# Kernel tuning notes

Measured on AMD Instinct MI355X. Metric: run time of the kernel, lower is better.

The kernel has to match this reference:

```python
import jax, jax.numpy as jnp
import numpy as np

B, T, N, F, U, K = 64, 96, 64, 64, 64, 2
M = 2 * K + 1  # num_matrices = len(supports)*K + 1
NUM_CLASSES, NUM_PATIENT = 4, 50


def diffusion_conv(x, supports, W, b, K):
    # x: (B, N, Fin). Faithful to DiffusionGraphConv incl. x1,x0 = x2,x1 carryover.
    xs = [x]
    x0 = x
    for S in supports:
        x1 = jnp.einsum('mn,bnf->bmf', S, x0)
        xs.append(x1)
        for _ in range(2, K + 1):
            x2 = 2.0 * jnp.einsum('mn,bnf->bmf', S, x1) - x0
            xs.append(x2)
            x1, x0 = x2, x1
    Bv, Nv, Fv = x.shape
    xcat = jnp.stack(xs, axis=-1).reshape(Bv, Nv, Fv * len(xs))  # feature-major, matrix-minor
    return xcat @ W + b


def dcgru_step(x, h, supports, Wg, bg, Wc, bc, K, units):
    cat = jnp.concatenate([x, h], axis=-1)
    ru = jax.nn.sigmoid(diffusion_conv(cat, supports, Wg, bg, K))
    r, u = ru[..., :units], ru[..., units:]
    c = jnp.tanh(diffusion_conv(jnp.concatenate([x, r * h], axis=-1), supports, Wc, bc, K))
    return u * h + (1.0 - u) * c


def encoder(inputs, supports, layer_params, K, units):
    # inputs: (T, B, N, Fin); returns last-layer outputs over time (T, B, N, units)
    cur = inputs
    for (Wg, bg, Wc, bc) in layer_params:
        h0 = jnp.zeros((cur.shape[1], cur.shape[2], units), cur.dtype)
        def step(h, x, Wg=Wg, bg=bg, Wc=Wc, bc=bc):
            hn = dcgru_step(x, h, supports, Wg, bg, Wc, bc, K, units)
            return hn, hn
        _, cur = jax.lax.scan(step, h0, cur)
    return cur


def setup_inputs() -> dict:
    key = jax.random.key(0)
    ks = jax.random.split(key, 20)
    def w(k, shape):
        return (jax.random.normal(k, shape, dtype=jnp.float32) / np.sqrt(shape[0])).astype(jnp.float32)
    def rw(k):  # row-normalized random-walk support
        A = jax.random.uniform(k, (N, N), dtype=jnp.float32)
        return A / jnp.sum(A, axis=1, keepdims=True)
    in0 = F + U   # layer 0 concat(x, h)
    in1 = U + U   # layer 1
    inp = {
        'input_seq': jax.random.normal(ks[0], (B, T, N, F), dtype=jnp.float32),
        'seq_lengths': jax.random.randint(ks[1], (B,), 1, T + 1, dtype=jnp.int32),
        'support0': rw(ks[2]),
        'support1': rw(ks[3]),
        'Wg0': w(ks[4], (in0 * M, 2 * U)), 'bg0': jnp.ones((2 * U,), jnp.float32),
        'Wc0': w(ks[5], (in0 * M, U)),     'bc0': jnp.zeros((U,), jnp.float32),
        'Wg1': w(ks[6], (in1 * M, 2 * U)), 'bg1': jnp.ones((2 * U,), jnp.float32),
        'Wc1': w(ks[7], (in1 * M, U)),     'bc1': jnp.zeros((U,), jnp.float32),
        'fc_w': w(ks[8], (U, NUM_CLASSES)), 'fc_b': jnp.zeros((NUM_CLASSES,), jnp.float32),
        'id_w': w(ks[9], (U, NUM_PATIENT)), 'id_b': jnp.zeros((NUM_PATIENT,), jnp.float32),
    }
    return inp


def reference(input_seq, seq_lengths, support0, support1,
              Wg0, bg0, Wc0, bc0, Wg1, bg1, Wc1, bc1,
              fc_w, fc_b, id_w, id_b):
    supports = [support0, support1]
    layer_params = [(Wg0, bg0, Wc0, bc0), (Wg1, bg1, Wc1, bc1)]
    inputs = jnp.transpose(input_seq, (1, 0, 2, 3))        # (T, B, N, F)
    outs = encoder(inputs, supports, layer_params, K, U)    # (T, B, N, U)
    out_bt = jnp.transpose(outs, (1, 0, 2, 3))              # (B, T, N, U)
    last = out_bt[jnp.arange(out_bt.shape[0]), seq_lengths - 1]  # (B, N, U)
    h = jax.nn.relu(last)  # dropout is identity in eval
    pool_seizure = jnp.max(h @ fc_w + fc_b, axis=1)         # max over nodes -> (B, num_classes)
    pool_identity = jnp.max(h @ id_w + id_b, axis=1)        # (B, num_patient)
    return pool_seizure, pool_identity
```

## Files before the change

### kernel.cpp

```cpp
#include <hip/hip_runtime.h>


#define GN 81920
#define CN 40960
#define WS_NEED ((4*GN + 4*CN) * 2)

#define OFF_T0  0
#define OFF_T1  33792
#define OFF_T2  67584
#define OFF_S0H 101376
#define OFF_S0L 110080
#define OFF_S1H 118784
#define OFF_S1L 127488
#define OFF_HB  136192
#define OFF_BG  153088
#define OFF_BC  154112
#define OFF_CTL 154624
#define SMEM_SZ 154640

#define RSS 68
#define RSHB 66

#define TA(node, feat) ((node) * 132 + ((feat) ^ ((((node) >> 3) & 7) << 3)))

typedef __attribute__((ext_vector_type(4))) short s4v;
typedef __attribute__((ext_vector_type(8))) short s8v;
typedef __attribute__((ext_vector_type(4))) float f4v;

#define MFMA16(a, b, c) __builtin_amdgcn_mfma_f32_16x16x32_bf16((a), (b), (c), 0, 0, 0)

__device__ __forceinline__ float dcr_b2f(unsigned short x) {
  return __uint_as_float(((unsigned)x) << 16);
}
__device__ __forceinline__ unsigned short dcr_f2b(float x) {
  unsigned u = __float_as_uint(x);
  u += 0x7fffu + ((u >> 16) & 1u);
  return (unsigned short)(u >> 16);
}
__device__ __forceinline__ unsigned dcr_pack(float v) {
  unsigned short hh = dcr_f2b(v);
  unsigned short hl = dcr_f2b(v - dcr_b2f(hh));
  return ((unsigned)hl << 16) | (unsigned)hh;
}
__device__ __forceinline__ float dcr_rdw(unsigned w) {
  return dcr_b2f((unsigned short)w) + dcr_b2f((unsigned short)(w >> 16));
}
__device__ __forceinline__ float dcr_ld(const void* p, int idx, int isf) {
  if (isf) return ((const float*)p)[idx];
  return dcr_b2f(((const unsigned short*)p)[idx]);
}
__device__ __forceinline__ float dcr_sigm(float x) {
  return 1.0f / (1.0f + __expf(-x));
}
__device__ __forceinline__ float dcr_tanh(float x) {
  return 2.0f / (1.0f + __expf(-2.0f * x)) - 1.0f;
}
__device__ __forceinline__ s8v dcr_ld8(const unsigned short* p) {
  s8v r;
  *(s4v*)&r = *(const s4v*)p;
  *((s4v*)&r + 1) = *(const s4v*)(p + 4);
  return r;
}

#define UNPACK8(AH, AL, TP, NODE, KB)                                      \
  {                                                                        \
    const int a0_ = TA(NODE, KB);                                          \
    uint4 q0_ = *(const uint4*)((TP) + a0_);                               \
    uint4 q1_ = *(const uint4*)((TP) + a0_ + 4);                           \
    AH[0] = (short)(q0_.x); AL[0] = (short)(q0_.x >> 16);                  \
    AH[1] = (short)(q0_.y); AL[1] = (short)(q0_.y >> 16);                  \
    AH[2] = (short)(q0_.z); AL[2] = (short)(q0_.z >> 16);                  \
    AH[3] = (short)(q0_.w); AL[3] = (short)(q0_.w >> 16);                  \
    AH[4] = (short)(q1_.x); AL[4] = (short)(q1_.x >> 16);                  \
    AH[5] = (short)(q1_.y); AL[5] = (short)(q1_.y >> 16);                  \
    AH[6] = (short)(q1_.z); AL[6] = (short)(q1_.z >> 16);                  \
    AH[7] = (short)(q1_.w); AL[7] = (short)(q1_.w >> 16);                  \
  }

__global__ void dcr_repack(const void* wg0, const void* wc0,
                           const void* wg1, const void* wc1,
                           const void* s0, unsigned short* o) {
  __shared__ int sisf;
  if (threadIdx.x == 0) {
    const unsigned short* ss = (const unsigned short*)s0;
    int hits = 0;
    for (int i = 0; i < 32; ++i) {
      unsigned hb = ((unsigned)ss[2 * i] >> 8) & 0xFFu;
      if (hb >= 0x30u && hb <= 0x3Fu) ++hits;
    }
    sisf = (hits < 16) ? 1 : 0;
  }
  __syncthreads();
  const int isf = sisf;
  const int NT = 4 * GN + 4 * CN;
  for (int e = blockIdx.x * blockDim.x + threadIdx.x; e < NT;
       e += gridDim.x * blockDim.x) {
    const void* W;
    int pl, ee, ncol, m, nt, ks, lane, j;
    if (e < 4 * GN) {
      int li = e / (2 * GN);
      int rem = e - li * 2 * GN;
      pl = rem / GN;
      ee = rem - pl * GN;
      W = li ? wg1 : wg0;
      ncol = 128;
      j = ee & 7; lane = (ee >> 3) & 63; ks = (ee >> 9) & 3;
      nt = (ee >> 11) & 7; m = ee >> 14;
    } else {
      int c = e - 4 * GN;
      int li = c / (2 * CN);
      int rem = c - li * 2 * CN;
      pl = rem / CN;
      ee = rem - pl * CN;
      W = li ? wc1 : wc0;
      ncol = 64;
      j = ee & 7; lane = (ee >> 3) & 63; ks = (ee >> 9) & 3;
      nt = (ee >> 11) & 3; m = ee >> 13;
    }
    if (pl == 1 && !isf) continue;
    const int f = ks * 32 + ((lane >> 4) & 3) * 8 + j;
    const int col = nt * 16 + (lane & 15);
    const int si = (f * 5 + m) * ncol + col;
    unsigned short v;
    if (!isf) {
      v = ((const unsigned short*)W)[si];
    } else {
      float w = ((const float*)W)[si];
      unsigned short hh = dcr_f2b(w);
      v = (pl == 0) ? hh : dcr_f2b(w - dcr_b2f(hh));
    }
    o[e] = v;
  }
}

__device__ __forceinline__ void dcr_gp(
    f4v& A0, f4v& A1, f4v& A2, f4v& A3,
    f4v& A4, f4v& A5, f4v& A6, f4v& A7,
    const unsigned* T, const unsigned short* rph, const unsigned short* rpl,
    int m, int w, int lane, int wlo) {
  const int ln15 = lane & 15;
  const int k8 = ((lane >> 4) & 3) * 8;
#pragma unroll
  for (int ks = 0; ks < 4; ++ks) {
    const int fo0 = (((m * 8 + w * 2 + 0) * 4 + ks) * 64 + lane) * 8;
    const int fo1 = (((m * 8 + w * 2 + 1) * 4 + ks) * 64 + lane) * 8;
    s8v bh0 = dcr_ld8(rph + fo0);
    s8v bh1 = dcr_ld8(rph + fo1);
    s8v bl0, bl1;
    if (wlo) { bl0 = dcr_ld8(rpl + fo0); bl1 = dcr_ld8(rpl + fo1); }
    const int kb = ks * 32 + k8;
#define DCR_GPM(AX, AY, MT)                                                \
    {                                                                      \
      const int node = (MT) * 16 + ln15;                                   \
      s8v ah, al;                                                          \
      UNPACK8(ah, al, T, node, kb)                                         \
      AX = MFMA16(ah, bh0, AX);                                            \
      AX = MFMA16(al, bh0, AX);                                            \
      if (wlo) AX = MFMA16(ah, bl0, AX);                                   \
      AY = MFMA16(ah, bh1, AY);                                            \
      AY = MFMA16(al, bh1, AY);                                            \
      if (wlo) AY = MFMA16(ah, bl1, AY);                                   \
    }
    DCR_GPM(A0, A4, 0)
    DCR_GPM(A1, A5, 1)
    DCR_GPM(A2, A6, 2)
    DCR_GPM(A3, A7, 3)
#undef DCR_GPM
  }
}

__device__ __forceinline__ void dcr_cp(f4v& A0, f4v& A1, f4v& A2, f4v& A3,
                                       const unsigned* T,
                                       const unsigned short* rph,
                                       const unsigned short* rpl,
                                       int m, int w4, int lane, int wlo,
                                       int pass) {
  const int ln15 = lane & 15;
  const int k8 = ((lane >> 4) & 3) * 8;
#pragma unroll
  for (int ks2 = 0; ks2 < 2; ++ks2) {
    const int ks = pass * 2 + ks2;
    const int fo = (((m * 4 + w4) * 4 + ks) * 64 + lane) * 8;
    s8v bh = dcr_ld8(rph + fo);
    s8v bl;
    if (wlo) bl = dcr_ld8(rpl + fo);
    const int kb = ks2 * 32 + k8;
#define DCR_CPM(AX, MT)                                                    \
    {                                                                      \
      const int node = (MT) * 16 + ln15;                                   \
      s8v ah, al;                                                          \
      UNPACK8(ah, al, T, node, kb)                                         \
      AX = MFMA16(ah, bh, AX);                                             \
      AX = MFMA16(al, bh, AX);                                             \
      if (wlo) AX = MFMA16(ah, bl, AX);                                    \
    }
    DCR_CPM(A0, 0)
    DCR_CPM(A1, 1)
    DCR_CPM(A2, 2)
    DCR_CPM(A3, 3)
#undef DCR_CPM
  }
}

#define DCR_API(ACX, J)                                                    \
  {                                                                        \
    if (ih_) {                                                             \
      _Pragma("unroll") for (int r = 0; r < 4; ++r)                        \
        ACX[r] = -0.5f * dcr_rdw(ih_[TA(orow + rq + r, fb + (J) * 16)]);   \
    } else {                                                               \
      ACX[0] = 0.0f; ACX[1] = 0.0f; ACX[2] = 0.0f; ACX[3] = 0.0f;          \
    }                                                                      \
  }
#define DCR_APM(ACX, J)                                                    \
  {                                                                        \
    s8v bh, b2;                                                            \
    _Pragma("unroll") for (int j = 0; j < 8; ++j) {                        \
      const unsigned w_ = src[TA(kb + j, fb + (J) * 16)];                  \
      bh[j] = (short)w_;                                                   \
      b2[j] = (short)(w_ >> 16);                                           \
    }                                                                      \
    ACX = MFMA16(ah, bh, ACX);                                             \
    ACX = MFMA16(ah, b2, ACX);                                             \
    if (wlo) ACX = MFMA16(al, bh, ACX);                                    \
  }
#define DCR_APS(ACX, J)                                                    \
  {                                                                        \
    _Pragma("unroll") for (int r = 0; r < 4; ++r)                          \
      dst[TA(orow + rq + r, fb + (J) * 16)] = dcr_pack(fct * ACX[r]);      \
  }

template <int NMT>
__device__ __forceinline__ void dcr_ap(const unsigned short* sh_,
                                       const unsigned short* sl_,
                                       const unsigned* src, unsigned* dst,
                                       const unsigned* ih_,
                                       int idx, int nmt0, int lane, int wlo) {
  const int ln15 = lane & 15;
  const int k8 = ((lane >> 4) & 3) * 8;
  const int rq = ((lane >> 4) & 3) * 4;
  const int orow = idx * 16;
  const int fb = nmt0 * 16 + ln15;
  f4v AC0, AC1, AC2, AC3;
  DCR_API(AC0, 0)
  DCR_API(AC1, 1)
  if constexpr (NMT == 4) {
    DCR_API(AC2, 2)
    DCR_API(AC3, 3)
  }
#pragma unroll
  for (int ks = 0; ks < 2; ++ks) {
    const int kb = ks * 32 + k8;
    s8v ah = dcr_ld8(sh_ + (orow + ln15) * RSS + kb);
    s8v al;
    if (wlo) al = dcr_ld8(sl_ + (orow + ln15) * RSS + kb);
    DCR_APM(AC0, 0)
    DCR_APM(AC1, 1)
    if constexpr (NMT == 4) {
      DCR_APM(AC2, 2)
      DCR_APM(AC3, 3)
    }
  }
  const float fct = ih_ ? 2.0f : 1.0f;
  DCR_APS(AC0, 0)
  DCR_APS(AC1, 1)
  if constexpr (NMT == 4) {
    DCR_APS(AC2, 2)
    DCR_APS(AC3, 3)
  }
}

template <int L>
__device__ __forceinline__ void dcr_layer(
    f4v& hA0, f4v& hA1, f4v& hA2, f4v& hA3,
    f4v& hB0, f4v& hB1, f4v& hB2, f4v& hB3,
    const void* xseq, int b, int t, int isf, int wlo,
    const unsigned short* rp,
    unsigned* T0, unsigned* T1, unsigned* T2,
    const unsigned short* S0h, const unsigned short* S0l,
    const unsigned short* S1h, const unsigned short* S1l,
    unsigned* HB, const float* BG, const float* BC,
    int tid, int lane, int wid) {
  const int ln15 = lane & 15;
  const int rq = ((lane >> 4) & 3) * 4;
  const unsigned short* rpgh = rp + (L * 2 + 0) * GN;
  const unsigned short* rpgl = rp + (L * 2 + 1) * GN;
  const unsigned short* rpch = rp + 4 * GN + (L * 2 + 0) * CN;
  const unsigned short* rpcl = rp + 4 * GN + (L * 2 + 1) * CN;

  f4v A0 = {0.0f, 0.0f, 0.0f, 0.0f}, A1 = A0, A2 = A0, A3 = A0;
  f4v A4 = A0, A5 = A0, A6 = A0, A7 = A0;

  if (wid < 4) dcr_gp(A0, A1, A2, A3, A4, A5, A6, A7, T0, rpgh, rpgl, 0, wid, lane, wlo);
  else if (wid >= 8 && wid < 12) dcr_cp(A0, A1, A2, A3, T0, rpch, rpcl, 0, wid - 8, lane, wlo, 0);
  else dcr_ap<4>(S0h, S0l, T0, T1, nullptr, wid & 3, (wid < 8) ? 4 : 0, lane, wlo);
  __syncthreads();
  if (wid < 4) dcr_gp(A0, A1, A2, A3, A4, A5, A6, A7, T1, rpgh, rpgl, 1, wid, lane, wlo);
  else if (wid >= 8 && wid < 12) dcr_cp(A0, A1, A2, A3, T1, rpch, rpcl, 1, wid - 8, lane, wlo, 0);
  else dcr_ap<4>(S0h, S0l, T1, T2, T0, wid & 3, (wid < 8) ? 4 : 0, lane, wlo);
  __syncthreads();
  if (wid < 4) dcr_gp(A0, A1, A2, A3, A4, A5, A6, A7, T2, rpgh, rpgl, 2, wid, lane, wlo);
  else if (wid >= 8 && wid < 12) dcr_cp(A0, A1, A2, A3, T2, rpch, rpcl, 2, wid - 8, lane, wlo, 0);
  else dcr_ap<4>(S1h, S1l, T1, T0, nullptr, wid & 3, (wid < 8) ? 4 : 0, lane, wlo);
  __syncthreads();
  if (wid < 4) dcr_gp(A0, A1, A2, A3, A4, A5, A6, A7, T0, rpgh, rpgl, 3, wid, lane, wlo);
  else if (wid >= 8 && wid < 12) dcr_cp(A0, A1, A2, A3, T0, rpch, rpcl, 3, wid - 8, lane, wlo, 0);
  else dcr_ap<4>(S1h, S1l, T0, T2, T1, wid & 3, (wid < 8) ? 4 : 0, lane, wlo);
  __syncthreads();

  if (wid < 4) {
    dcr_gp(A0, A1, A2, A3, A4, A5, A6, A7, T2, rpgh, rpgl, 4, wid, lane, wlo);
    const int g0 = wid * 32 + ln15;
    const float bg0v = BG[L * 128 + g0];
    const float bg1v = BG[L * 128 + g0 + 16];
#define DCR_GF(AX, AY, MT)                                                 \
    { _Pragma("unroll") for (int r = 0; r < 4; ++r) {                      \
        const int node = (MT) * 16 + rq + r;                               \
        const float s0_ = dcr_sigm(AX[r] + bg0v);                          \
        const float s1_ = dcr_sigm(AY[r] + bg1v);                          \
        if (wid < 2) {                                                     \
          const float h0_ = dcr_rdw(HB[node * RSHB + g0]);                 \
          const float h1_ = dcr_rdw(HB[node * RSHB + g0 + 16]);            \
          T0[TA(node, g0)] = dcr_pack(s0_ * h0_);                          \
          T0[TA(node, g0 + 16)] = dcr_pack(s1_ * h1_);                     \
        } else {                                                           \
          T1[TA(node, g0)] = dcr_pack(s0_);                                \
          T1[TA(node, g0 + 16)] = dcr_pack(s1_);                           \
        } } }
    DCR_GF(A0, A4, 0)
    DCR_GF(A1, A5, 1)
    DCR_GF(A2, A6, 2)
    DCR_GF(A3, A7, 3)
#undef DCR_GF
  } else if (wid >= 8 && wid < 12) {
    dcr_cp(A0, A1, A2, A3, T2, rpch, rpcl, 4, wid - 8, lane, wlo, 0);
  }
  __syncthreads();

  if (wid >= 8 && wid < 12) dcr_cp(A0, A1, A2, A3, T0, rpch, rpcl, 0, wid - 8, lane, wlo, 1);
  else if (wid >= 4) dcr_ap<2>(S0h, S0l, T0, T1, nullptr, wid & 3, (wid < 8) ? 2 : 0, lane, wlo);
  __syncthreads();
  if (wid >= 8 && wid < 12) dcr_cp(A0, A1, A2, A3, T1, rpch, rpcl, 1, wid - 8, lane, wlo, 1);
  else if (wid >= 4) dcr_ap<2>(S0h, S0l, T1, T2, T0, wid & 3, (wid < 8) ? 2 : 0, lane, wlo);
  __syncthreads();
  if (wid >= 8 && wid < 12) dcr_cp(A0, A1, A2, A3, T2, rpch, rpcl, 2, wid - 8, lane, wlo, 1);
  else if (wid >= 4) dcr_ap<2>(S1h, S1l, T1, T0, nullptr, wid & 3, (wid < 8) ? 2 : 0, lane, wlo);
  __syncthreads();
  if (wid >= 8 && wid < 12) dcr_cp(A0, A1, A2, A3, T0, rpch, rpcl, 3, wid - 8, lane, wlo, 1);
  else if (wid >= 4) dcr_ap<2>(S1h, S1l, T0, T1, T1, wid & 3, (wid < 8) ? 2 : 0, lane, wlo);
  __syncthreads();

  if (wid >= 8 && wid < 12) {
    dcr_cp(A0, A1, A2, A3, T1, rpch, rpcl, 4, wid - 8, lane, wlo, 1);
    const int f = (wid - 8) * 16 + ln15;
    const float bcv = BC[L * 64 + f];
#define DCR_CF(AX, HX, MT)                                                 \
    { _Pragma("unroll") for (int r = 0; r < 4; ++r) {                      \
        const int node = (MT) * 16 + rq + r;                               \
        const float c = dcr_tanh(AX[r] + bcv);                             \
        const float u = dcr_rdw(T1[TA(node, 64 + f)]);                     \
        HX[r] = u * HX[r] + (1.0f - u) * c; } }
    if constexpr (L == 0) {
      DCR_CF(A0, hA0, 0)
      DCR_CF(A1, hA1, 1)
      DCR_CF(A2, hA2, 2)
      DCR_CF(A3, hA3, 3)
#define DCR_SG0(HAX, HBX, MT)                                              \
      { _Pragma("unroll") for (int r = 0; r < 4; ++r) {                    \
          const int node = (MT) * 16 + rq + r;                             \
          T0[TA(node, f)] = dcr_pack(HAX[r]);                              \
          const unsigned pw = dcr_pack(HBX[r]);                            \
          T0[TA(node, 64 + f)] = pw;                                       \
          HB[node * RSHB + f] = pw; } }
      DCR_SG0(hA0, hB0, 0)
      DCR_SG0(hA1, hB1, 1)
      DCR_SG0(hA2, hB2, 2)
      DCR_SG0(hA3, hB3, 3)
#undef DCR_SG0
    } else {
      DCR_CF(A0, hB0, 0)
      DCR_CF(A1, hB1, 1)
      DCR_CF(A2, hB2, 2)
      DCR_CF(A3, hB3, 3)
#define DCR_SG1(HAX, MT)                                                   \
      { _Pragma("unroll") for (int r = 0; r < 4; ++r) {                    \
          const int node = (MT) * 16 + rq + r;                             \
          const unsigned pw = dcr_pack(HAX[r]);                            \
          T0[TA(node, 64 + f)] = pw;                                       \
          HB[node * RSHB + f] = pw; } }
      DCR_SG1(hA0, 0)
      DCR_SG1(hA1, 1)
      DCR_SG1(hA2, 2)
      DCR_SG1(hA3, 3)
#undef DCR_SG1
    }
#undef DCR_CF
  } else if (L == 1 && wid < 8) {
    const int tn = (t < 95) ? (t + 1) : 95;
    const int n = tid >> 3;
    const int f0 = (tid & 7) * 8;
    const int xo = (b * 96 + tn) * 4096 + n * 64 + f0;
    const int base = TA(n, f0);
    uint4 q0, q1;
    if (isf) {
      const float* xp = (const float*)xseq + xo;
      q0.x = dcr_pack(xp[0]); q0.y = dcr_pack(xp[1]);
      q0.z = dcr_pack(xp[2]); q0.w = dcr_pack(xp[3]);
      q1.x = dcr_pack(xp[4]); q1.y = dcr_pack(xp[5]);
      q1.z = dcr_pack(xp[6]); q1.w = dcr_pack(xp[7]);
    } else {
      const unsigned short* xp = (const unsigned short*)xseq + xo;
      s8v v = *(const s8v*)xp;
      q0.x = (unsigned)(unsigned short)v[0];
      q0.y = (unsigned)(unsigned short)v[1];
      q0.z = (unsigned)(unsigned short)v[2];
      q0.w = (unsigned)(unsigned short)v[3];
      q1.x = (unsigned)(unsigned short)v[4];
      q1.y = (unsigned)(unsigned short)v[5];
      q1.z = (unsigned)(unsigned short)v[6];
      q1.w = (unsigned)(unsigned short)v[7];
    }
    *(uint4*)(T0 + base) = q0;
    *(uint4*)(T0 + base + 4) = q1;
  }
  __syncthreads();
}

__global__ __launch_bounds__(1024)
__attribute__((amdgpu_waves_per_eu(4, 4)))
void dcr_mfma(
    const void* xseq, const void* s0, const void* s1,
    const void* bg0, const void* bg1,
    const void* p64a, const void* p64b, const void* p64c,
    const void* fcw, const void* fcb, const void* idw, const void* idb,
    const unsigned short* rp, void* outp) {
  extern __shared__ char sm[];
  unsigned* const T0 = (unsigned*)(sm + OFF_T0);
  unsigned* const T1 = (unsigned*)(sm + OFF_T1);
  unsigned* const T2 = (unsigned*)(sm + OFF_T2);
  unsigned short* const S0h = (unsigned short*)(sm + OFF_S0H);
  unsigned short* const S0l = (unsigned short*)(sm + OFF_S0L);
  unsigned short* const S1h = (unsigned short*)(sm + OFF_S1H);
  unsigned short* const S1l = (unsigned short*)(sm + OFF_S1L);
  unsigned* const HB = (unsigned*)(sm + OFF_HB);
  float* const BG = (float*)(sm + OFF_BG);
  float* const BC = (float*)(sm + OFF_BC);
  int* const ctl = (int*)(sm + OFF_CTL);

  const int tid = threadIdx.x;
  const int b = blockIdx.x;
  const int lane = tid & 63;
  const int wid = tid >> 6;

  if (tid == 0) {
    const unsigned short* ss = (const unsigned short*)s0;
    int hits = 0;
    for (int i = 0; i < 32; ++i) {
      unsigned hb = ((unsigned)ss[2 * i] >> 8) & 0xFFu;
      if (hb >= 0x30u && hb <= 0x3Fu) ++hits;
    }
    int isf_ = (hits < 16) ? 1 : 0;
    int sel = 0;
    {
      const unsigned* w = (const unsigned*)p64a;
      unsigned any = 0;
      for (int i = 0; i < 16; ++i) any |= w[i];
      if (!any) {
        sel = 1;
        const unsigned* w1 = (const unsigned*)p64b;
        unsigned any1 = 0;
        for (int i = 0; i < 16; ++i) any1 |= w1[i];
        if (!any1) sel = 2;
      }
    }
    const unsigned* w =
        (const unsigned*)(sel == 0 ? p64a : (sel == 1 ? p64b : p64c));
    int i64 = 1;
    for (int i = 0; i < 8; ++i)
      if (w[2 * i + 1] != 0u) i64 = 0;
    ctl[0] = isf_;
    ctl[1] = sel;
    ctl[2] = i64;
  }
  __syncthreads();
  const int isf = ctl[0];
  const int sel = ctl[1];
  const int i64 = ctl[2];
  const int wlo = isf;
  const void* seqp = (sel == 0) ? p64a : (sel == 1 ? p64b : p64c);
  const void* bcA = (sel == 0) ? p64b : p64a;
  const void* bcB = (sel == 2) ? p64b : p64c;

  for (int i = 0; i < 4; ++i) {
    const int flat = i * 1024 + tid;
    const int out = flat >> 6, in = flat & 63;
    float v0, v1;
    if (isf) {
      v0 = ((const float*)s0)[flat];
      v1 = ((const float*)s1)[flat];
    } else {
      v0 = dcr_b2f(((const unsigned short*)s0)[flat]);
      v1 = dcr_b2f(((const unsigned short*)s1)[flat]);
    }
    unsigned short hh = dcr_f2b(v0);
    S0h[out * RSS + in] = hh;
    S0l[out * RSS + in] = dcr_f2b(v0 - dcr_b2f(hh));
    hh = dcr_f2b(v1);
    S1h[out * RSS + in] = hh;
    S1l[out * RSS + in] = dcr_f2b(v1 - dcr_b2f(hh));
  }
  if (tid < 128) {
    BG[tid] = dcr_ld(bg0, tid, isf);
    BG[128 + tid] = dcr_ld(bg1, tid, isf);
  } else if (tid < 192) {
    const int j = tid - 128;
    BC[j] = dcr_ld(bcA, j, isf);
    BC[64 + j] = dcr_ld(bcB, j, isf);
  }

  int tl_;
  if (i64) tl_ = (int)((const long long*)seqp)[b] - 1;
  else     tl_ = ((const int*)seqp)[b] - 1;
  if (tl_ < 0) tl_ = 0;
  if (tl_ > 95) tl_ = 95;

  f4v hA0 = {0.0f, 0.0f, 0.0f, 0.0f}, hA1 = hA0, hA2 = hA0, hA3 = hA0;
  f4v hB0 = hA0, hB1 = hA0, hB2 = hA0, hB3 = hA0;

  const int ln15 = lane & 15;
  const int rq = ((lane >> 4) & 3) * 4;

  if (wid < 8) {
    const int n = tid >> 3;
    const int f0 = (tid & 7) * 8;
    const int xo = (b * 96 + 0) * 4096 + n * 64 + f0;
    const int base = TA(n, f0);
    uint4 q0, q1;
    if (isf) {
      const float* xp = (const float*)xseq + xo;
      q0.x = dcr_pack(xp[0]); q0.y = dcr_pack(xp[1]);
      q0.z = dcr_pack(xp[2]); q0.w = dcr_pack(xp[3]);
      q1.x = dcr_pack(xp[4]); q1.y = dcr_pack(xp[5]);
      q1.z = dcr_pack(xp[6]); q1.w = dcr_pack(xp[7]);
    } else {
      const unsigned short* xp = (const unsigned short*)xseq + xo;
      s8v v = *(const s8v*)xp;
      q0.x = (unsigned)(unsigned short)v[0];
      q0.y = (unsigned)(unsigned short)v[1];
      q0.z = (unsigned)(unsigned short)v[2];
      q0.w = (unsigned)(unsigned short)v[3];
      q1.x = (unsigned)(unsigned short)v[4];
      q1.y = (unsigned)(unsigned short)v[5];
      q1.z = (unsigned)(unsigned short)v[6];
      q1.w = (unsigned)(unsigned short)v[7];
    }
    *(uint4*)(T0 + base) = q0;
    *(uint4*)(T0 + base + 4) = q1;
  } else if (wid < 12) {
    const int f = (wid - 8) * 16 + ln15;
#pragma unroll
    for (int mt = 0; mt < 4; ++mt)
#pragma unroll
      for (int r = 0; r < 4; ++r) {
        const int node = mt * 16 + rq + r;
        T0[TA(node, 64 + f)] = 0u;
        HB[node * RSHB + f] = 0u;
      }
  }
  __syncthreads();

  for (int t = 0; t < 96; ++t) {
    dcr_layer<0>(hA0, hA1, hA2, hA3, hB0, hB1, hB2, hB3,
                 xseq, b, t, isf, wlo, rp, T0, T1, T2,
                 S0h, S0l, S1h, S1l, HB, BG, BC, tid, lane, wid);
    dcr_layer<1>(hA0, hA1, hA2, hA3, hB0, hB1, hB2, hB3,
                 xseq, b, t, isf, wlo, rp, T0, T1, T2,
                 S0h, S0l, S1h, S1l, HB, BG, BC, tid, lane, wid);
    if (t == tl_) break;
  }

  __syncthreads();
  float* const hx = (float*)(sm + OFF_T0);
  float* const hw = (float*)(sm + OFF_T1);
  float* const red = (float*)(sm + OFF_T2);
  if (wid >= 8 && wid < 12) {
    const int f = (wid - 8) * 16 + ln15;
#define DCR_HX(HX, MT)                                                     \
    { _Pragma("unroll") for (int r = 0; r < 4; ++r) {                      \
        const int node = (MT) * 16 + rq + r;                               \
        hx[node * 66 + f] = fmaxf(HX[r], 0.0f); } }
    DCR_HX(hB0, 0)
    DCR_HX(hB1, 1)
    DCR_HX(hB2, 2)
    DCR_HX(hB3, 3)
#undef DCR_HX
  }
  {
    const int u = tid >> 4;
    for (int c = (tid & 15); c < 54; c += 16)
      hw[u * 56 + c] = (c < 4) ? dcr_ld(fcw, u * 4 + c, isf)
                               : dcr_ld(idw, u * 50 + (c - 4), isf);
  }
  __syncthreads();
  if (tid < 864) {
    const int c = tid % 54, nb = tid / 54;
    float mx = -3.4e38f;
    for (int nn = nb * 4; nn < nb * 4 + 4; ++nn) {
      float s = 0.0f;
#pragma unroll 8
      for (int uu = 0; uu < 64; ++uu) s += hx[nn * 66 + uu] * hw[uu * 56 + c];
      mx = fmaxf(mx, s);
    }
    red[nb * 54 + c] = mx;
  }
  __syncthreads();
  if (tid < 54) {
    float mx = red[tid];
#pragma unroll
    for (int g = 1; g < 16; ++g) mx = fmaxf(mx, red[g * 54 + tid]);
    mx += (tid < 4) ? dcr_ld(fcb, tid, isf) : dcr_ld(idb, tid - 4, isf);
    const int o = (tid < 4) ? (b * 4 + tid) : (256 + b * 50 + (tid - 4));
    if (isf) ((float*)outp)[o] = mx;
    else     ((unsigned short*)outp)[o] = dcr_f2b(mx);
  }
}

__device__ void dcr_proj(float* aG, float* aC, const float (*buf)[68],
                         const void* Wg, const void* Wc, int m, int fh,
                         int n, int fb, int doG, int doC, int isf) {
  if (!isf) {
    const unsigned* G = (const unsigned*)Wg;
    const unsigned* C = (const unsigned*)Wc;
    const int fd = fb >> 1;
#pragma unroll 4
    for (int k = 0; k < 64; ++k) {
      float xk = buf[n][k];
      int row = (fh + k) * 5 + m;
      if (doG) {
        const unsigned* wr = G + row * 64 + fd;
        unsigned p0 = wr[0], p1 = wr[1], p2 = wr[32], p3 = wr[33];
        aG[0] += xk * __uint_as_float(p0 << 16);
        aG[1] += xk * __uint_as_float(p0 & 0xFFFF0000u);
        aG[2] += xk * __uint_as_float(p1 << 16);
        aG[3] += xk * __uint_as_float(p1 & 0xFFFF0000u);
        aG[4] += xk * __uint_as_float(p2 << 16);
        aG[5] += xk * __uint_as_float(p2 & 0xFFFF0000u);
        aG[6] += xk * __uint_as_float(p3 << 16);
        aG[7] += xk * __uint_as_float(p3 & 0xFFFF0000u);
      }
      if (doC) {
        const unsigned* wr = C + row * 32 + fd;
        unsigned p0 = wr[0], p1 = wr[1];
        aC[0] += xk * __uint_as_float(p0 << 16);
        aC[1] += xk * __uint_as_float(p0 & 0xFFFF0000u);
        aC[2] += xk * __uint_as_float(p1 << 16);
        aC[3] += xk * __uint_as_float(p1 & 0xFFFF0000u);
      }
    }
  } else {
    const float* G = (const float*)Wg;
    const float* C = (const float*)Wc;
#pragma unroll 4
    for (int k = 0; k < 64; ++k) {
      float xk = buf[n][k];
      int row = (fh + k) * 5 + m;
      if (doG) {
        const float* wr = G + row * 128 + fb;
#pragma unroll
        for (int j = 0; j < 4; ++j) {
          aG[j] += xk * wr[j];
          aG[4 + j] += xk * wr[64 + j];
        }
      }
      if (doC) {
        const float* wr = C + row * 64 + fb;
#pragma unroll
        for (int j = 0; j < 4; ++j) aC[j] += xk * wr[j];
      }
    }
  }
}

__device__ void dcr_apply(float (*dst)[68], const float (*src)[68],
                          const unsigned short (*sS)[65], int n, int fb,
                          int cheb) {
  float a0 = 0.0f, a1 = 0.0f, a2 = 0.0f, a3 = 0.0f;
#pragma unroll 8
  for (int m = 0; m < 64; ++m) {
    float s = dcr_b2f(sS[n][m]);
    float4 v = *(const float4*)(&src[m][fb]);
    a0 += s * v.x;
    a1 += s * v.y;
    a2 += s * v.z;
    a3 += s * v.w;
  }
  if (cheb) {
    dst[n][fb + 0] = 2.0f * a0 - dst[n][fb + 0];
    dst[n][fb + 1] = 2.0f * a1 - dst[n][fb + 1];
    dst[n][fb + 2] = 2.0f * a2 - dst[n][fb + 2];
    dst[n][fb + 3] = 2.0f * a3 - dst[n][fb + 3];
  } else {
    dst[n][fb + 0] = a0;
    dst[n][fb + 1] = a1;
    dst[n][fb + 2] = a2;
    dst[n][fb + 3] = a3;
  }
}

__device__ void dcr_half(float* aG, float* aC, const void* Wg, const void* Wc,
                         int fh, int doG, int doC, float (*xa)[68],
                         float (*xb)[68], const unsigned short (*sS0)[65],
                         const unsigned short (*sS1)[65], int n, int fb,
                         int isf) {
  dcr_proj(aG, aC, xa, Wg, Wc, 0, fh, n, fb, doG, doC, isf);
  dcr_apply(xb, xa, sS0, n, fb, 0);
  __syncthreads();
  dcr_proj(aG, aC, xb, Wg, Wc, 1, fh, n, fb, doG, doC, isf);
  dcr_apply(xa, xb, sS0, n, fb, 1);
  __syncthreads();
  dcr_proj(aG, aC, xa, Wg, Wc, 2, fh, n, fb, doG, doC, isf);
  __syncthreads();
  dcr_apply(xa, xb, sS1, n, fb, 0);
  __syncthreads();
  dcr_proj(aG, aC, xa, Wg, Wc, 3, fh, n, fb, doG, doC, isf);
  dcr_apply(xb, xa, sS1, n, fb, 1);
  __syncthreads();
  dcr_proj(aG, aC, xb, Wg, Wc, 4, fh, n, fb, doG, doC, isf);
  __syncthreads();
}

__global__ __launch_bounds__(1024) void dcr_scalar(
    const void* xseq, const void* s0, const void* s1, const void* wg0,
    const void* wc0, const void* wg1, const void* wc1, const void* bg0,
    const void* bg1, const void* p64a, const void* p64b, const void* p64c,
    const void* fcw, const void* fcb, const void* idw, const void* idb,
    void* outp) {
  __shared__ float xa[64][68];
  __shared__ float xb[64][68];
  __shared__ unsigned short sS[2][64][65];
  __shared__ float bGs[2][128];
  __shared__ float bCs[2][64];
  __shared__ float red[16][54];
  __shared__ int ctl[4];

  const int tid = threadIdx.x;
  const int b = blockIdx.x;
  const int n = tid >> 4;
  const int fb = (tid & 15) * 4;

  if (tid == 0) {
    const unsigned short* ss = (const unsigned short*)s0;
    int hits = 0;
    for (int i = 0; i < 32; ++i) {
      unsigned hb = ((unsigned)ss[2 * i] >> 8) & 0xFFu;
      if (hb >= 0x30u && hb <= 0x3Fu) ++hits;
    }
    int isf = (hits < 16) ? 1 : 0;
    int sel = 0;
    {
      const unsigned* w = (const unsigned*)p64a;
      unsigned any = 0;
      for (int i = 0; i < 16; ++i) any |= w[i];
      if (!any) {
        sel = 1;
        const unsigned* w1 = (const unsigned*)p64b;
        unsigned any1 = 0;
        for (int i = 0; i < 16; ++i) any1 |= w1[i];
        if (!any1) sel = 2;
      }
    }
    const unsigned* w =
        (const unsigned*)(sel == 0 ? p64a : (sel == 1 ? p64b : p64c));
    int i64 = 1;
    for (int i = 0; i < 8; ++i)
      if (w[2 * i + 1] != 0u) i64 = 0;
    ctl[0] = isf;
    ctl[1] = sel;
    ctl[2] = i64;
  }
  __syncthreads();
  const int isf = ctl[0];
  const int sel = ctl[1];
  const int i64 = ctl[2];
  const void* seqp = (sel == 0) ? p64a : (sel == 1 ? p64b : p64c);
  const void* bcA = (sel == 0) ? p64b : p64a;
  const void* bcB = (sel == 2) ? p64b : p64c;

  for (int i = 0; i < 4; ++i) {
    int flat = i * 1024 + tid;
    int nn = flat >> 6, mm = flat & 63;
    unsigned short v0, v1;
    if (isf) {
      v0 = dcr_f2b(((const float*)s0)[flat]);
      v1 = dcr_f2b(((const float*)s1)[flat]);
    } else {
      v0 = ((const unsigned short*)s0)[flat];
      v1 = ((const unsigned short*)s1)[flat];
    }
    sS[0][nn][mm] = v0;
    sS[1][nn][mm] = v1;
  }
  if (tid < 128) {
    bGs[0][tid] = dcr_ld(bg0, tid, isf);
    bGs[1][tid] = dcr_ld(bg1, tid, isf);
  } else if (tid < 192) {
    int j = tid - 128;
    bCs[0][j] = dcr_ld(bcA, j, isf);
    bCs[1][j] = dcr_ld(bcB, j, isf);
  }

  int tl;
  if (i64) tl = (int)((const long long*)seqp)[b] - 1;
  else     tl = ((const int*)seqp)[b] - 1;
  if (tl < 0) tl = 0;
  if (tl > 95) tl = 95;

  float h0r[4], h1r[4];
#pragma unroll
  for (int j = 0; j < 4; ++j) {
    h0r[j] = 0.0f;
    h1r[j] = 0.0f;
  }
  __syncthreads();

  for (int t = 0; t < 96; ++t) {
    {
      float aG[8], aC[4];
#pragma unroll
      for (int j = 0; j < 8; ++j) aG[j] = 0.0f;
#pragma unroll
      for (int j = 0; j < 4; ++j) aC[j] = 0.0f;
      int xoff = (b * 96 + t) * 4096 + n * 64 + fb;
#pragma unroll
      for (int j = 0; j < 4; ++j) xa[n][fb + j] = dcr_ld(xseq, xoff + j, isf);
      __syncthreads();
      dcr_half(aG, aC, wg0, wc0, 0, 1, 1, xa, xb, sS[0], sS[1], n, fb, isf);
#pragma unroll
      for (int j = 0; j < 4; ++j) xa[n][fb + j] = h0r[j];
      __syncthreads();
      dcr_half(aG, aC, wg0, wc0, 64, 1, 0, xa, xb, sS[0], sS[1], n, fb, isf);
      float rr[4], uu[4];
#pragma unroll
      for (int j = 0; j < 4; ++j) {
        rr[j] = dcr_sigm(aG[j] + bGs[0][fb + j]);
        uu[j] = dcr_sigm(aG[4 + j] + bGs[0][64 + fb + j]);
      }
#pragma unroll
      for (int j = 0; j < 4; ++j) xa[n][fb + j] = rr[j] * h0r[j];
      __syncthreads();
      dcr_half(aG, aC, wg0, wc0, 64, 0, 1, xa, xb, sS[0], sS[1], n, fb, isf);
#pragma unroll
      for (int j = 0; j < 4; ++j) {
        float c = dcr_tanh(aC[j] + bCs[0][fb + j]);
        h0r[j] = uu[j] * h0r[j] + (1.0f - uu[j]) * c;
      }
    }
    {
      float aG[8], aC[4];
#pragma unroll
      for (int j = 0; j < 8; ++j) aG[j] = 0.0f;
#pragma unroll
      for (int j = 0; j < 4; ++j) aC[j] = 0.0f;
#pragma unroll
      for (int j = 0; j < 4; ++j) xa[n][fb + j] = h0r[j];
      __syncthreads();
      dcr_half(aG, aC, wg1, wc1, 0, 1, 1, xa, xb, sS[0], sS[1], n, fb, isf);
#pragma unroll
      for (int j = 0; j < 4; ++j) xa[n][fb + j] = h1r[j];
      __syncthreads();
      dcr_half(aG, aC, wg1, wc1, 64, 1, 0, xa, xb, sS[0], sS[1], n, fb, isf);
      float rr[4], uu[4];
#pragma unroll
      for (int j = 0; j < 4; ++j) {
        rr[j] = dcr_sigm(aG[j] + bGs[1][fb + j]);
        uu[j] = dcr_sigm(aG[4 + j] + bGs[1][64 + fb + j]);
      }
#pragma unroll
      for (int j = 0; j < 4; ++j) xa[n][fb + j] = rr[j] * h1r[j];
      __syncthreads();
      dcr_half(aG, aC, wg1, wc1, 64, 0, 1, xa, xb, sS[0], sS[1], n, fb, isf);
#pragma unroll
      for (int j = 0; j < 4; ++j) {
        float c = dcr_tanh(aC[j] + bCs[1][fb + j]);
        h1r[j] = uu[j] * h1r[j] + (1.0f - uu[j]) * c;
      }
    }
    if (t == tl) break;
  }

  __syncthreads();
#pragma unroll
  for (int j = 0; j < 4; ++j) xa[n][fb + j] = fmaxf(h1r[j], 0.0f);
  {
    int u = tid >> 4;
    for (int c = (tid & 15); c < 54; c += 16)
      xb[u][c] = (c < 4) ? dcr_ld(fcw, u * 4 + c, isf)
                         : dcr_ld(idw, u * 50 + (c - 4), isf);
  }
  __syncthreads();
  if (tid < 864) {
    int c = tid % 54, nb = tid / 54;
    float mx = -3.4e38f;
    for (int nn = nb * 4; nn < nb * 4 + 4; ++nn) {
      float s = 0.0f;
#pragma unroll 8
      for (int u = 0; u < 64; ++u) s += xa[nn][u] * xb[u][c];
      mx = fmaxf(mx, s);
    }
    red[nb][c] = mx;
  }
  __syncthreads();
  if (tid < 54) {
    float mx = red[0][tid];
#pragma unroll
    for (int g = 1; g < 16; ++g) mx = fmaxf(mx, red[g][tid]);
    mx += (tid < 4) ? dcr_ld(fcb, tid, isf) : dcr_ld(idb, tid - 4, isf);
    int o = (tid < 4) ? (b * 4 + tid) : (256 + b * 50 + (tid - 4));
    if (isf) ((float*)outp)[o] = mx;
    else     ((unsigned short*)outp)[o] = dcr_f2b(mx);
  }
}

static int dcr_find_nth(const int* s, int n, int sz, int nth) {
  int c = 0;
  for (int i = 0; i < n; ++i)
    if (s[i] == sz) {
      if (c == nth) return i;
      ++c;
    }
  return -1;
}

extern "C" void kernel_launch(void* const* d_in, const int* in_sizes, int n_in,
                              void* d_out, int out_size, void* d_ws,
                              size_t ws_size, hipStream_t stream) {
  (void)out_size;
  int i_seq = dcr_find_nth(in_sizes, n_in, 393216, 0);
  int i_s0 = dcr_find_nth(in_sizes, n_in, 4096, 0);
  int i_s1 = dcr_find_nth(in_sizes, n_in, 4096, 1);
  int i_wg0 = dcr_find_nth(in_sizes, n_in, 81920, 0);
  int i_wg1 = dcr_find_nth(in_sizes, n_in, 81920, 1);
  int i_wc0 = dcr_find_nth(in_sizes, n_in, 40960, 0);
  int i_wc1 = dcr_find_nth(in_sizes, n_in, 40960, 1);
  int i_bg0 = dcr_find_nth(in_sizes, n_in, 128, 0);
  int i_bg1 = dcr_find_nth(in_sizes, n_in, 128, 1);
  int i_64a = dcr_find_nth(in_sizes, n_in, 64, 0);
  int i_64b = dcr_find_nth(in_sizes, n_in, 64, 1);
  int i_64c = dcr_find_nth(in_sizes, n_in, 64, 2);
  int i_fcw = dcr_find_nth(in_sizes, n_in, 256, 0);
  int i_fcb = dcr_find_nth(in_sizes, n_in, 4, 0);
  int i_idw = dcr_find_nth(in_sizes, n_in, 3200, 0);
  int i_idb = dcr_find_nth(in_sizes, n_in, 50, 0);
  if (i_seq < 0 || i_s0 < 0 || i_s1 < 0 || i_wg0 < 0 || i_wg1 < 0 ||
      i_wc0 < 0 || i_wc1 < 0 || i_bg0 < 0 || i_bg1 < 0 || i_64a < 0 ||
      i_64b < 0 || i_64c < 0 || i_fcw < 0 || i_fcb < 0 || i_idw < 0 ||
      i_idb < 0) {
    i_seq = 0;  i_64a = 1;  i_s0 = 2;   i_s1 = 3;
    i_wg0 = 4;  i_bg0 = 5;  i_wc0 = 6;  i_64b = 7;
    i_wg1 = 8;  i_bg1 = 9;  i_wc1 = 10; i_64c = 11;
    i_fcw = 12; i_fcb = 13; i_idw = 14; i_idb = 15;
  }

  if (d_ws == nullptr || ws_size < (size_t)WS_NEED) {
    dcr_scalar<<<dim3(64), dim3(1024), 0, stream>>>(
        d_in[i_seq], d_in[i_s0], d_in[i_s1], d_in[i_wg0], d_in[i_wc0],
        d_in[i_wg1], d_in[i_wc1], d_in[i_bg0], d_in[i_bg1], d_in[i_64a],
        d_in[i_64b], d_in[i_64c], d_in[i_fcw], d_in[i_fcb], d_in[i_idw],
        d_in[i_idb], d_out);
    return;
  }

  dcr_repack<<<dim3(256), dim3(256), 0, stream>>>(
      d_in[i_wg0], d_in[i_wc0], d_in[i_wg1], d_in[i_wc1], d_in[i_s0],
      (unsigned short*)d_ws);

  static bool attr_set = false;
  if (!attr_set) {
    (void)hipFuncSetAttribute((const void*)dcr_mfma,
                              hipFuncAttributeMaxDynamicSharedMemorySize,
                              SMEM_SZ);
    attr_set = true;
  }

  dcr_mfma<<<dim3(64), dim3(1024), SMEM_SZ, stream>>>(
      d_in[i_seq], d_in[i_s0], d_in[i_s1], d_in[i_bg0], d_in[i_bg1],
      d_in[i_64a], d_in[i_64b], d_in[i_64c], d_in[i_fcw], d_in[i_fcb],
      d_in[i_idw], d_in[i_idb], (const unsigned short*)d_ws, d_out);
}
```

Baseline: 10.62 ms.

## Rebalance warp roles and shorten candidate-phase diffusion schedule by one barrier

Gate projection now uses eight warps, each handling one 16-column tile instead of four warps with two tiles. The support-propagation work moves to the remaining four warps, each doing eight tiles. The candidate-gate diffusion chain is rescheduled so the S0 and S1 second-order steps run in parallel in one phase, writing into the upper half of a tile buffer through new offset parameters. This removes one synchronization phase per layer step, but it changes buffer aliasing (r*h now goes to T1, u stays in T1) and raises register pressure in the eight-tile propagation path.

```diff
diff --git a/kernel.cpp b/kernel.cpp
--- a/kernel.cpp
+++ b/kernel.cpp
@@ -133,39 +133,33 @@
   }
 }
 
-__device__ __forceinline__ void dcr_gp(
+__device__ __forceinline__ void dcr_gp1(
     f4v& A0, f4v& A1, f4v& A2, f4v& A3,
-    f4v& A4, f4v& A5, f4v& A6, f4v& A7,
     const unsigned* T, const unsigned short* rph, const unsigned short* rpl,
     int m, int w, int lane, int wlo) {
   const int ln15 = lane & 15;
   const int k8 = ((lane >> 4) & 3) * 8;
 #pragma unroll
   for (int ks = 0; ks < 4; ++ks) {
-    const int fo0 = (((m * 8 + w * 2 + 0) * 4 + ks) * 64 + lane) * 8;
-    const int fo1 = (((m * 8 + w * 2 + 1) * 4 + ks) * 64 + lane) * 8;
-    s8v bh0 = dcr_ld8(rph + fo0);
-    s8v bh1 = dcr_ld8(rph + fo1);
-    s8v bl0, bl1;
-    if (wlo) { bl0 = dcr_ld8(rpl + fo0); bl1 = dcr_ld8(rpl + fo1); }
+    const int fo = (((m * 8 + w) * 4 + ks) * 64 + lane) * 8;
+    s8v bh = dcr_ld8(rph + fo);
+    s8v bl;
+    if (wlo) bl = dcr_ld8(rpl + fo);
     const int kb = ks * 32 + k8;
-#define DCR_GPM(AX, AY, MT)                                                \
+#define DCR_G1(AX, MT)                                                     \
     {                                                                      \
       const int node = (MT) * 16 + ln15;                                   \
       s8v ah, al;                                                          \
       UNPACK8(ah, al, T, node, kb)                                         \
-      AX = MFMA16(ah, bh0, AX);                                            \
-      AX = MFMA16(al, bh0, AX);                                            \
-      if (wlo) AX = MFMA16(ah, bl0, AX);                                   \
-      AY = MFMA16(ah, bh1, AY);                                            \
-      AY = MFMA16(al, bh1, AY);                                            \
-      if (wlo) AY = MFMA16(ah, bl1, AY);                                   \
-    }
-    DCR_GPM(A0, A4, 0)
-    DCR_GPM(A1, A5, 1)
-    DCR_GPM(A2, A6, 2)
-    DCR_GPM(A3, A7, 3)
-#undef DCR_GPM
+      AX = MFMA16(ah, bh, AX);                                             \
+      AX = MFMA16(al, bh, AX);                                             \
+      if (wlo) AX = MFMA16(ah, bl, AX);                                    \
+    }
+    DCR_G1(A0, 0)
+    DCR_G1(A1, 1)
+    DCR_G1(A2, 2)
+    DCR_G1(A3, 3)
+#undef DCR_G1
   }
 }
 
@@ -174,7 +168,7 @@
                                        const unsigned short* rph,
                                        const unsigned short* rpl,
                                        int m, int w4, int lane, int wlo,
-                                       int pass) {
+                                       int pass, int tof) {
   const int ln15 = lane & 15;
   const int k8 = ((lane >> 4) & 3) * 8;
 #pragma unroll
@@ -189,7 +183,7 @@
     {                                                                      \
       const int node = (MT) * 16 + ln15;                                   \
       s8v ah, al;                                                          \
-      UNPACK8(ah, al, T, node, kb)                                         \
+      UNPACK8(ah, al, T, node, tof + kb)                                   \
       AX = MFMA16(ah, bh, AX);                                             \
       AX = MFMA16(al, bh, AX);                                             \
       if (wlo) AX = MFMA16(ah, bl, AX);                                    \
@@ -206,7 +200,8 @@
   {                                                                        \
     if (ih_) {                                                             \
       _Pragma("unroll") for (int r = 0; r < 4; ++r)                        \
-        ACX[r] = -0.5f * dcr_rdw(ih_[TA(orow + rq + r, fb + (J) * 16)]);   \
+        ACX[r] = -0.5f *                                                   \
+                 dcr_rdw(ih_[TA(orow + rq + r, iof + fb + (J) * 16)]);     \
     } else {                                                               \
       ACX[0] = 0.0f; ACX[1] = 0.0f; ACX[2] = 0.0f; ACX[3] = 0.0f;          \
     }                                                                      \
@@ -215,7 +210,7 @@
   {                                                                        \
     s8v bh, b2;                                                            \
     _Pragma("unroll") for (int j = 0; j < 8; ++j) {                        \
-      const unsigned w_ = src[TA(kb + j, fb + (J) * 16)];                  \
+      const unsigned w_ = src[TA(kb + j, sof + fb + (J) * 16)];            \
       bh[j] = (short)w_;                                                   \
       b2[j] = (short)(w_ >> 16);                                           \
     }                                                                      \
@@ -226,7 +221,8 @@
 #define DCR_APS(ACX, J)                                                    \
   {                                                                        \
     _Pragma("unroll") for (int r = 0; r < 4; ++r)                          \
-      dst[TA(orow + rq + r, fb + (J) * 16)] = dcr_pack(fct * ACX[r]);      \
+      dst[TA(orow + rq + r, dof + fb + (J) * 16)] =                        \
+          dcr_pack(fct * ACX[r]);                                          \
   }
 
 template <int NMT>
@@ -234,18 +230,25 @@
                                        const unsigned short* sl_,
                                        const unsigned* src, unsigned* dst,
                                        const unsigned* ih_,
+                                       int sof, int iof, int dof,
                                        int idx, int nmt0, int lane, int wlo) {
   const int ln15 = lane & 15;
   const int k8 = ((lane >> 4) & 3) * 8;
   const int rq = ((lane >> 4) & 3) * 4;
   const int orow = idx * 16;
   const int fb = nmt0 * 16 + ln15;
-  f4v AC0, AC1, AC2, AC3;
+  f4v AC0, AC1, AC2, AC3, AC4, AC5, AC6, AC7;
   DCR_API(AC0, 0)
   DCR_API(AC1, 1)
-  if constexpr (NMT == 4) {
+  if constexpr (NMT >= 4) {
     DCR_API(AC2, 2)
     DCR_API(AC3, 3)
+  }
+  if constexpr (NMT == 8) {
+    DCR_API(AC4, 4)
+    DCR_API(AC5, 5)
+    DCR_API(AC6, 6)
+    DCR_API(AC7, 7)
   }
 #pragma unroll
   for (int ks = 0; ks < 2; ++ks) {
@@ -255,17 +258,29 @@
     if (wlo) al = dcr_ld8(sl_ + (orow + ln15) * RSS + kb);
     DCR_APM(AC0, 0)
     DCR_APM(AC1, 1)
-    if constexpr (NMT == 4) {
+    if constexpr (NMT >= 4) {
       DCR_APM(AC2, 2)
       DCR_APM(AC3, 3)
+    }
+    if constexpr (NMT == 8) {
+      DCR_APM(AC4, 4)
+      DCR_APM(AC5, 5)
+      DCR_APM(AC6, 6)
+      DCR_APM(AC7, 7)
     }
   }
   const float fct = ih_ ? 2.0f : 1.0f;
   DCR_APS(AC0, 0)
   DCR_APS(AC1, 1)
-  if constexpr (NMT == 4) {
+  if constexpr (NMT >= 4) {
     DCR_APS(AC2, 2)
     DCR_APS(AC3, 3)
+  }
+  if constexpr (NMT == 8) {
+    DCR_APS(AC4, 4)
+    DCR_APS(AC5, 5)
+    DCR_APS(AC6, 6)
+    DCR_APS(AC7, 7)
   }
 }
 
@@ -288,69 +303,59 @@
   const unsigned short* rpcl = rp + 4 * GN + (L * 2 + 1) * CN;
 
   f4v A0 = {0.0f, 0.0f, 0.0f, 0.0f}, A1 = A0, A2 = A0, A3 = A0;
-  f4v A4 = A0, A5 = A0, A6 = A0, A7 = A0;
-
-  if (wid < 4) dcr_gp(A0, A1, A2, A3, A4, A5, A6, A7, T0, rpgh, rpgl, 0, wid, lane, wlo);
-  else if (wid >= 8 && wid < 12) dcr_cp(A0, A1, A2, A3, T0, rpch, rpcl, 0, wid - 8, lane, wlo, 0);
-  else dcr_ap<4>(S0h, S0l, T0, T1, nullptr, wid & 3, (wid < 8) ? 4 : 0, lane, wlo);
-  __syncthreads();
-  if (wid < 4) dcr_gp(A0, A1, A2, A3, A4, A5, A6, A7, T1, rpgh, rpgl, 1, wid, lane, wlo);
-  else if (wid >= 8 && wid < 12) dcr_cp(A0, A1, A2, A3, T1, rpch, rpcl, 1, wid - 8, lane, wlo, 0);
-  else dcr_ap<4>(S0h, S0l, T1, T2, T0, wid & 3, (wid < 8) ? 4 : 0, lane, wlo);
-  __syncthreads();
-  if (wid < 4) dcr_gp(A0, A1, A2, A3, A4, A5, A6, A7, T2, rpgh, rpgl, 2, wid, lane, wlo);
-  else if (wid >= 8 && wid < 12) dcr_cp(A0, A1, A2, A3, T2, rpch, rpcl, 2, wid - 8, lane, wlo, 0);
-  else dcr_ap<4>(S1h, S1l, T1, T0, nullptr, wid & 3, (wid < 8) ? 4 : 0, lane, wlo);
-  __syncthreads();
-  if (wid < 4) dcr_gp(A0, A1, A2, A3, A4, A5, A6, A7, T0, rpgh, rpgl, 3, wid, lane, wlo);
-  else if (wid >= 8 && wid < 12) dcr_cp(A0, A1, A2, A3, T0, rpch, rpcl, 3, wid - 8, lane, wlo, 0);
-  else dcr_ap<4>(S1h, S1l, T0, T2, T1, wid & 3, (wid < 8) ? 4 : 0, lane, wlo);
-  __syncthreads();
-
-  if (wid < 4) {
-    dcr_gp(A0, A1, A2, A3, A4, A5, A6, A7, T2, rpgh, rpgl, 4, wid, lane, wlo);
-    const int g0 = wid * 32 + ln15;
-    const float bg0v = BG[L * 128 + g0];
-    const float bg1v = BG[L * 128 + g0 + 16];
-#define DCR_GF(AX, AY, MT)                                                 \
+
+  if (wid < 8) dcr_gp1(A0, A1, A2, A3, T0, rpgh, rpgl, 0, wid, lane, wlo);
+  else if (wid < 12) dcr_cp(A0, A1, A2, A3, T0, rpch, rpcl, 0, wid - 8, lane, wlo, 0, 0);
+  else dcr_ap<8>(S0h, S0l, T0, T1, nullptr, 0, 0, 0, wid - 12, 0, lane, wlo);
+  __syncthreads();
+  if (wid < 8) dcr_gp1(A0, A1, A2, A3, T1, rpgh, rpgl, 1, wid, lane, wlo);
+  else if (wid < 12) dcr_cp(A0, A1, A2, A3, T1, rpch, rpcl, 1, wid - 8, lane, wlo, 0, 0);
+  else dcr_ap<8>(S0h, S0l, T1, T2, T0, 0, 0, 0, wid - 12, 0, lane, wlo);
+  __syncthreads();
+  if (wid < 8) dcr_gp1(A0, A1, A2, A3, T2, rpgh, rpgl, 2, wid, lane, wlo);
+  else if (wid < 12) dcr_cp(A0, A1, A2, A3, T2, rpch, rpcl, 2, wid - 8, lane, wlo, 0, 0);
+  else dcr_ap<8>(S1h, S1l, T1, T0, nullptr, 0, 0, 0, wid - 12, 0, lane, wlo);
+  __syncthreads();
+  if (wid < 8) dcr_gp1(A0, A1, A2, A3, T0, rpgh, rpgl, 3, wid, lane, wlo);
+  else if (wid < 12) dcr_cp(A0, A1, A2, A3, T0, rpch, rpcl, 3, wid - 8, lane, wlo, 0, 0);
+  else dcr_ap<8>(S1h, S1l, T0, T2, T1, 0, 0, 0, wid - 12, 0, lane, wlo);
+  __syncthreads();
+  if (wid < 8) {
+    dcr_gp1(A0, A1, A2, A3, T2, rpgh, rpgl, 4, wid, lane, wlo);
+    const int g = wid * 16 + ln15;
+    const float bgv = BG[L * 128 + g];
+#define DCR_GF(AX, MT)                                                     \
     { _Pragma("unroll") for (int r = 0; r < 4; ++r) {                      \
         const int node = (MT) * 16 + rq + r;                               \
-        const float s0_ = dcr_sigm(AX[r] + bg0v);                          \
-        const float s1_ = dcr_sigm(AY[r] + bg1v);                          \
-        if (wid < 2) {                                                     \
-          const float h0_ = dcr_rdw(HB[node * RSHB + g0]);                 \
-          const float h1_ = dcr_rdw(HB[node * RSHB + g0 + 16]);            \
-          T0[TA(node, g0)] = dcr_pack(s0_ * h0_);                          \
-          T0[TA(node, g0 + 16)] = dcr_pack(s1_ * h1_);                     \
+        const float s_ = dcr_sigm(AX[r] + bgv);                            \
+        if (wid < 4) {                                                     \
+          const float h_ = dcr_rdw(HB[node * RSHB + g]);                   \
+          T1[TA(node, g)] = dcr_pack(s_ * h_);                             \
         } else {                                                           \
-          T1[TA(node, g0)] = dcr_pack(s0_);                                \
-          T1[TA(node, g0 + 16)] = dcr_pack(s1_);                           \
+          T1[TA(node, g)] = dcr_pack(s_);                                  \
         } } }
-    DCR_GF(A0, A4, 0)
-    DCR_GF(A1, A5, 1)
-    DCR_GF(A2, A6, 2)
-    DCR_GF(A3, A7, 3)
+    DCR_GF(A0, 0)
+    DCR_GF(A1, 1)
+    DCR_GF(A2, 2)
+    DCR_GF(A3, 3)
 #undef DCR_GF
-  } else if (wid >= 8 && wid < 12) {
-    dcr_cp(A0, A1, A2, A3, T2, rpch, rpcl, 4, wid - 8, lane, wlo, 0);
-  }
-  __syncthreads();
-
-  if (wid >= 8 && wid < 12) dcr_cp(A0, A1, A2, A3, T0, rpch, rpcl, 0, wid - 8, lane, wlo, 1);
-  else if (wid >= 4) dcr_ap<2>(S0h, S0l, T0, T1, nullptr, wid & 3, (wid < 8) ? 2 : 0, lane, wlo);
-  __syncthreads();
-  if (wid >= 8 && wid < 12) dcr_cp(A0, A1, A2, A3, T1, rpch, rpcl, 1, wid - 8, lane, wlo, 1);
-  else if (wid >= 4) dcr_ap<2>(S0h, S0l, T1, T2, T0, wid & 3, (wid < 8) ? 2 : 0, lane, wlo);
-  __syncthreads();
-  if (wid >= 8 && wid < 12) dcr_cp(A0, A1, A2, A3, T2, rpch, rpcl, 2, wid - 8, lane, wlo, 1);
-  else if (wid >= 4) dcr_ap<2>(S1h, S1l, T1, T0, nullptr, wid & 3, (wid < 8) ? 2 : 0, lane, wlo);
-  __syncthreads();
-  if (wid >= 8 && wid < 12) dcr_cp(A0, A1, A2, A3, T0, rpch, rpcl, 3, wid - 8, lane, wlo, 1);
-  else if (wid >= 4) dcr_ap<2>(S1h, S1l, T0, T1, T1, wid & 3, (wid < 8) ? 2 : 0, lane, wlo);
-  __syncthreads();
-
+  } else if (wid < 12) {
+    dcr_cp(A0, A1, A2, A3, T2, rpch, rpcl, 4, wid - 8, lane, wlo, 0, 0);
+  }
+  __syncthreads();
+  if (wid < 8) dcr_ap<2>(S0h, S0l, T1, T2, nullptr, 0, 0, 0, wid & 3, (wid < 4) ? 0 : 2, lane, wlo);
+  else if (wid < 12) dcr_cp(A0, A1, A2, A3, T1, rpch, rpcl, 0, wid - 8, lane, wlo, 1, 0);
+  __syncthreads();
+  if (wid < 4) dcr_ap<4>(S0h, S0l, T2, T0, T1, 0, 0, 0, wid & 3, 0, lane, wlo);
+  else if (wid < 8) dcr_ap<4>(S1h, S1l, T2, T2, nullptr, 0, 0, 64, wid & 3, 0, lane, wlo);
+  else if (wid < 12) dcr_cp(A0, A1, A2, A3, T2, rpch, rpcl, 1, wid - 8, lane, wlo, 1, 0);
+  __syncthreads();
+  if (wid < 8) dcr_ap<2>(S1h, S1l, T2, T1, T2, 64, 0, 0, wid & 3, (wid < 4) ? 0 : 2, lane, wlo);
+  else if (wid < 12) dcr_cp(A0, A1, A2, A3, T0, rpch, rpcl, 2, wid - 8, lane, wlo, 1, 0);
+  __syncthreads();
   if (wid >= 8 && wid < 12) {
-    dcr_cp(A0, A1, A2, A3, T1, rpch, rpcl, 4, wid - 8, lane, wlo, 1);
+    dcr_cp(A0, A1, A2, A3, T2, rpch, rpcl, 3, wid - 8, lane, wlo, 1, 64);
+    dcr_cp(A0, A1, A2, A3, T1, rpch, rpcl, 4, wid - 8, lane, wlo, 1, 0);
     const int f = (wid - 8) * 16 + ln15;
     const float bcv = BC[L * 64 + f];
 #define DCR_CF(AX, HX, MT)                                                 \
```

Measured after the change: 10.34 ms. 2.6% less time.
